# Kernel tuning notes

Hardware: AMD Instinct MI355X
Metric: run time of the kernel (lower is better)

## Reference

```python
import jax, jax.numpy as jnp
import numpy as np


def _shift_lr(t):
    # t: [B, L, H] -> (left, right) neighbor states with zero padding
    B, L, H = t.shape
    pad = jnp.zeros((B, 1, H), dtype=t.dtype)
    left = jnp.concatenate([pad, t[:, :-1, :]], axis=1)
    right = jnp.concatenate([t[:, 1:, :], pad], axis=1)
    return left, right


def setup_inputs() -> dict:
    key = jax.random.key(0)
    ks = jax.random.split(key, 7)
    B, L, H = 32, 2048, 256
    h_t = jax.random.normal(ks[0], (B, L, H), dtype=jnp.float32)
    x = jax.random.normal(ks[1], (B, L, H), dtype=jnp.float32)
    h_slot = jax.random.normal(ks[2], (B, L, H), dtype=jnp.float32)
    h_intent = jax.random.normal(ks[3], (B, L, H), dtype=jnp.float32)
    c_t = jax.random.normal(ks[4], (B, L, H), dtype=jnp.float32)
    # gate order: [i, o, f, l, r, u]; linear in = 6H, out = H
    Ws = jax.random.normal(ks[5], (6, 6 * H, H), dtype=jnp.float32) * 0.02
    bs = jnp.zeros((6, H), dtype=jnp.float32)
    return {"h_t": h_t, "x": x, "h_slot": h_slot, "h_intent": h_intent,
            "c_t": c_t, "Ws": Ws, "bs": bs}


def reference(h_t, x, h_slot, h_intent, c_t, Ws, bs):
    h_left, h_right = _shift_lr(h_t)
    # concat order: [h_mid, h_left, h_right, x, h_slot, h_intent] -> [B,L,6H]
    cat = jnp.concatenate([h_t, h_left, h_right, x, h_slot, h_intent], axis=-1)
    # one batched GEMM for all six gates: [6, B, L, H]
    gates = jnp.einsum('blc,gch->gblh', cat, Ws) + bs[:, None, None, :]
    i_t = jax.nn.sigmoid(gates[0])
    o_t = jax.nn.sigmoid(gates[1])
    f_t = jax.nn.sigmoid(gates[2])
    l_t = jax.nn.sigmoid(gates[3])
    r_t = jax.nn.sigmoid(gates[4])
    u_t = jnp.tanh(gates[5])
    # softmax across the 4 gates (axis 0 of the stack)
    soft = jax.nn.softmax(jnp.stack([i_t, f_t, l_t, r_t], axis=0), axis=0)
    i_t, f_t, l_t, r_t = soft[0], soft[1], soft[2], soft[3]
    c_left, c_right = _shift_lr(c_t)
    c_new = f_t * c_t + l_t * c_left + r_t * c_right + i_t * u_t
    h_new = o_t * jnp.tanh(c_new)
    return (h_new, c_new)
```

## Files before the change

kernel.cpp:

```cpp
#include <hip/hip_runtime.h>

typedef __attribute__((ext_vector_type(8))) short short8;
typedef __attribute__((ext_vector_type(4))) float f32x4;

#define BB 32
#define LL 2048
#define HH 256
#define MTOT (BB*LL)
#define KK 1536
#define HSIZE (MTOT*HH)

__device__ __forceinline__ unsigned short f2bf(float f){
    unsigned u = __builtin_bit_cast(unsigned, f);
    u += 0x7FFFu + ((u >> 16) & 1u);
    return (unsigned short)(u >> 16);
}
__device__ __forceinline__ unsigned pk2(float lo, float hi){
    return (unsigned)f2bf(lo) | ((unsigned)f2bf(hi) << 16);
}
__device__ __forceinline__ float sigm(float v){
    return 1.0f / (1.0f + __expf(-v));
}
__device__ __forceinline__ float ftanh(float v){
    v = fminf(fmaxf(v, -30.0f), 30.0f);
    float e = __expf(2.0f * v);
    return (e - 1.0f) / (e + 1.0f);
}

__global__ __launch_bounds__(256) void prep_bt(const float* __restrict__ Ws,
                                               unsigned short* __restrict__ Bt){
    __shared__ float tile[64][65];
    int bid = blockIdx.x;
    int kb = bid % 24; int tmp = bid / 24; int hb = tmp & 3; int g = tmp >> 2;
    int t = threadIdx.x;
    const float* src = Ws + (size_t)g * (KK * HH) + (size_t)(kb * 64) * HH + hb * 64;
    #pragma unroll
    for (int it = 0; it < 16; ++it){
        int e = it * 256 + t; int kk = e >> 6, hh = e & 63;
        tile[kk][hh] = src[(size_t)kk * HH + hh];
    }
    __syncthreads();
    unsigned short* dst = Bt + (size_t)(g * 256 + hb * 64) * KK + kb * 64;
    #pragma unroll
    for (int it = 0; it < 16; ++it){
        int e = it * 256 + t; int hh = e >> 6, kk = e & 63;
        dst[(size_t)hh * KK + kk] = f2bf(tile[kk][hh]);
    }
}

__global__ __launch_bounds__(512, 2) void slstm_fused(
    const float* __restrict__ h_t, const float* __restrict__ x,
    const float* __restrict__ h_slot, const float* __restrict__ h_intent,
    const float* __restrict__ c_t, const float* __restrict__ bs,
    const unsigned short* __restrict__ Bt, float* __restrict__ out)
{
    __shared__ unsigned short As[128 * 40];
    __shared__ unsigned short Bs[384 * 40];

    const int t    = threadIdx.x;
    const int wv   = t >> 6,  ln  = t & 63;
    const int rg   = wv >> 2, ht  = wv & 3;
    const int quad = ln >> 4, l16 = ln & 15;

    const int h_chunk = blockIdx.x & 3;
    const int m_block = blockIdx.x >> 2;
    const int h0      = h_chunk * 64;

    const int  arow = t >> 2;
    const int  akq  = (t & 3) << 3;
    const long mg   = (long)m_block * 128 + arow;
    const int  lseq = (int)(mg & (LL - 1));

    f32x4 acc[4][6] = {};

    for (int ks = 0; ks < 48; ++ks){
        {
            int c  = ks >> 3;
            int kk = ((ks & 7) << 5) + akq;
            const float* src; int sh;
            switch (c){
                case 0:  src = h_t;      sh =  0; break;
                case 1:  src = h_t;      sh = -1; break;
                case 2:  src = h_t;      sh =  1; break;
                case 3:  src = x;        sh =  0; break;
                case 4:  src = h_slot;   sh =  0; break;
                default: src = h_intent; sh =  0; break;
            }
            int sl = lseq + sh;
            float4 v0 = make_float4(0.f,0.f,0.f,0.f), v1 = v0;
            if ((unsigned)sl < (unsigned)LL){
                const float* p = src + ((mg + sh) * HH + kk);
                v0 = *(const float4*)p;
                v1 = *(const float4*)(p + 4);
            }
            uint4 w;
            w.x = pk2(v0.x, v0.y); w.y = pk2(v0.z, v0.w);
            w.z = pk2(v1.x, v1.y); w.w = pk2(v1.z, v1.w);
            *(uint4*)&As[arow * 40 + akq] = w;
        }
        #pragma unroll
        for (int i = 0; i < 3; ++i){
            int s   = i * 512 + t;
            int col = s >> 2;
            int kq  = (s & 3) << 3;
            int g   = col >> 6, hc = col & 63;
            const uint4 bv = *(const uint4*)(Bt + (size_t)(g * 256 + h0 + hc) * KK + ks * 32 + kq);
            *(uint4*)&Bs[col * 40 + kq] = bv;
        }
        __syncthreads();
        short8 a[4];
        #pragma unroll
        for (int mt = 0; mt < 4; ++mt)
            a[mt] = *(const short8*)&As[(rg * 64 + mt * 16 + l16) * 40 + quad * 8];
        #pragma unroll
        for (int g = 0; g < 6; ++g){
            short8 bfrag = *(const short8*)&Bs[(g * 64 + ht * 16 + l16) * 40 + quad * 8];
            #pragma unroll
            for (int mt = 0; mt < 4; ++mt)
                acc[mt][g] = __builtin_amdgcn_mfma_f32_16x16x32_bf16(a[mt], bfrag, acc[mt][g], 0, 0, 0);
        }
        __syncthreads();
    }

    const int h = h0 + ht * 16 + l16;
    float bias[6];
    #pragma unroll
    for (int g = 0; g < 6; ++g) bias[g] = bs[g * HH + h];

    #pragma unroll
    for (int mt = 0; mt < 4; ++mt){
        #pragma unroll
        for (int r = 0; r < 4; ++r){
            long row = (long)m_block * 128 + rg * 64 + mt * 16 + quad * 4 + r;
            int  ls  = (int)(row & (LL - 1));
            float gi = sigm(acc[mt][0][r] + bias[0]);
            float go = sigm(acc[mt][1][r] + bias[1]);
            float gf = sigm(acc[mt][2][r] + bias[2]);
            float gl = sigm(acc[mt][3][r] + bias[3]);
            float gr = sigm(acc[mt][4][r] + bias[4]);
            float gu = ftanh(acc[mt][5][r] + bias[5]);
            float ei = __expf(gi), ef = __expf(gf), el = __expf(gl), er = __expf(gr);
            float inv = 1.0f / (ei + ef + el + er);
            float cm  = c_t[row * HH + h];
            float clv = (ls > 0)      ? c_t[(row - 1) * HH + h] : 0.0f;
            float crv = (ls < LL - 1) ? c_t[(row + 1) * HH + h] : 0.0f;
            float cn  = (ef * cm + el * clv + er * crv + ei * gu) * inv;
            float hn  = go * ftanh(cn);
            out[row * HH + h]         = hn;
            out[HSIZE + row * HH + h] = cn;
        }
    }
}

extern "C" void kernel_launch(void* const* d_in, const int* in_sizes, int n_in,
                              void* d_out, int out_size, void* d_ws, size_t ws_size,
                              hipStream_t stream){
    const float* h_t      = (const float*)d_in[0];
    const float* x        = (const float*)d_in[1];
    const float* h_slot   = (const float*)d_in[2];
    const float* h_intent = (const float*)d_in[3];
    const float* c_t      = (const float*)d_in[4];
    const float* Ws       = (const float*)d_in[5];
    const float* bs       = (const float*)d_in[6];
    unsigned short* Bt    = (unsigned short*)d_ws;

    prep_bt<<<576, 256, 0, stream>>>(Ws, Bt);
    slstm_fused<<<2048, 512, 0, stream>>>(h_t, x, h_slot, h_intent, c_t, bs, Bt, (float*)d_out);
}
```

Measured before the change: 990.7 us.

## Double-buffer GEMM tiles with direct global-to-LDS B loads and XOR swizzle

Reworks the fused sLSTM GEMM main loop into a double-buffered pipeline. The next K-slice of activations is loaded into registers and the next weight slice is issued with global_load_lds before the current slice's MFMAs run, leaving one barrier per iteration. The weight prep kernel now writes B pre-tiled and XOR-swizzled so each K-slice is a contiguous chunk, and LDS rows drop the padding in favour of a matching swizzle. Block indices are also remapped to group blocks that share weight chunks. LDS use doubles, which may reduce occupancy, and correctness depends on the swizzled layouts staying consistent between the prep and fused kernels.

```diff
diff --git a/kernel.cpp b/kernel.cpp
--- a/kernel.cpp
+++ b/kernel.cpp
@@ -10,6 +10,8 @@
 #define KK 1536
 #define HSIZE (MTOT*HH)
 
+#define SWZ4(v) (((v) & 3) ^ (((v) >> 2) & 3))
+
 __device__ __forceinline__ unsigned short f2bf(float f){
     unsigned u = __builtin_bit_cast(unsigned, f);
     u += 0x7FFFu + ((u >> 16) & 1u);
@@ -25,6 +27,11 @@
     v = fminf(fmaxf(v, -30.0f), 30.0f);
     float e = __expf(2.0f * v);
     return (e - 1.0f) / (e + 1.0f);
+}
+__device__ __forceinline__ void gload_lds16(const void* g, void* l){
+    __builtin_amdgcn_global_load_lds(
+        (const __attribute__((address_space(1))) unsigned int*)g,
+        (__attribute__((address_space(3))) unsigned int*)l, 16, 0, 0);
 }
 
 __global__ __launch_bounds__(256) void prep_bt(const float* __restrict__ Ws,
@@ -40,11 +47,21 @@
         tile[kk][hh] = src[(size_t)kk * HH + hh];
     }
     __syncthreads();
-    unsigned short* dst = Bt + (size_t)(g * 256 + hb * 64) * KK + kb * 64;
-    #pragma unroll
-    for (int it = 0; it < 16; ++it){
-        int e = it * 256 + t; int hh = e >> 6, kk = e & 63;
-        dst[(size_t)hh * KK + kk] = f2bf(tile[kk][hh]);
+    #pragma unroll
+    for (int it = 0; it < 2; ++it){
+        int jj  = t;
+        int ksl = it;
+        int hc  = jj >> 2, qp = jj & 3;
+        int col = g * 64 + hc;
+        int q   = qp ^ SWZ4(col);
+        int kbase = ksl * 32 + q * 8;
+        unsigned wz[4];
+        #pragma unroll
+        for (int p = 0; p < 4; ++p)
+            wz[p] = pk2(tile[kbase + 2*p][hc], tile[kbase + 2*p + 1][hc]);
+        int ksg = kb * 2 + ksl;
+        size_t off = ((size_t)(hb * 48 + ksg) * 1536 + (size_t)g * 256 + jj) * 8;
+        *(uint4*)&Bt[off] = *(uint4*)wz;
     }
 }
 
@@ -54,71 +71,91 @@
     const float* __restrict__ c_t, const float* __restrict__ bs,
     const unsigned short* __restrict__ Bt, float* __restrict__ out)
 {
-    __shared__ unsigned short As[128 * 40];
-    __shared__ unsigned short Bs[384 * 40];
+    __shared__ __align__(16) unsigned short As[2][128 * 32];
+    __shared__ __align__(16) unsigned short Bs[2][384 * 32];
 
     const int t    = threadIdx.x;
     const int wv   = t >> 6,  ln  = t & 63;
     const int rg   = wv >> 2, ht  = wv & 3;
     const int quad = ln >> 4, l16 = ln & 15;
 
-    const int h_chunk = blockIdx.x & 3;
-    const int m_block = blockIdx.x >> 2;
+    const int rawb = blockIdx.x;
+    const int vb   = (rawb & 7) * 256 + (rawb >> 3);
+    const int h_chunk = vb & 3;
+    const int m_block = vb >> 2;
     const int h0      = h_chunk * 64;
 
     const int  arow = t >> 2;
-    const int  akq  = (t & 3) << 3;
+    const int  aq   = t & 3;
+    const int  akq  = aq << 3;
     const long mg   = (long)m_block * 128 + arow;
     const int  lseq = (int)(mg & (LL - 1));
+    const int  awq  = (aq ^ SWZ4(arow)) << 3;
+    const int  qa   = (quad ^ SWZ4(l16)) << 3;
+
+    const unsigned short* BtH = Bt + (size_t)h_chunk * 48 * 1536 * 8;
 
     f32x4 acc[4][6] = {};
 
+    float4 av0, av1;
+    auto stageA_issue = [&](int ks){
+        int c  = ks >> 3;
+        int kk = ((ks & 7) << 5) + akq;
+        const float* src; int sh;
+        switch (c){
+            case 0:  src = h_t;      sh =  0; break;
+            case 1:  src = h_t;      sh = -1; break;
+            case 2:  src = h_t;      sh =  1; break;
+            case 3:  src = x;        sh =  0; break;
+            case 4:  src = h_slot;   sh =  0; break;
+            default: src = h_intent; sh =  0; break;
+        }
+        int sl = lseq + sh;
+        av0 = make_float4(0.f,0.f,0.f,0.f); av1 = av0;
+        if ((unsigned)sl < (unsigned)LL){
+            const float* p = src + ((mg + sh) * HH + kk);
+            av0 = *(const float4*)p;
+            av1 = *(const float4*)(p + 4);
+        }
+    };
+    auto stageB = [&](int buf, int ks){
+        const unsigned short* gsrc = BtH + (size_t)ks * 1536 * 8;
+        #pragma unroll
+        for (int i = 0; i < 3; ++i){
+            gload_lds16(gsrc + (size_t)(i * 512 + t) * 8,
+                        &Bs[buf][(i * 512 + wv * 64) * 8]);
+        }
+    };
+    auto stageA_write = [&](int buf){
+        uint4 w;
+        w.x = pk2(av0.x, av0.y); w.y = pk2(av0.z, av0.w);
+        w.z = pk2(av1.x, av1.y); w.w = pk2(av1.z, av1.w);
+        *(uint4*)&As[buf][arow * 32 + awq] = w;
+    };
+
+    stageA_issue(0);
+    stageB(0, 0);
+    stageA_write(0);
+    __syncthreads();
+
     for (int ks = 0; ks < 48; ++ks){
-        {
-            int c  = ks >> 3;
-            int kk = ((ks & 7) << 5) + akq;
-            const float* src; int sh;
-            switch (c){
-                case 0:  src = h_t;      sh =  0; break;
-                case 1:  src = h_t;      sh = -1; break;
-                case 2:  src = h_t;      sh =  1; break;
-                case 3:  src = x;        sh =  0; break;
-                case 4:  src = h_slot;   sh =  0; break;
-                default: src = h_intent; sh =  0; break;
-            }
-            int sl = lseq + sh;
-            float4 v0 = make_float4(0.f,0.f,0.f,0.f), v1 = v0;
-            if ((unsigned)sl < (unsigned)LL){
-                const float* p = src + ((mg + sh) * HH + kk);
-                v0 = *(const float4*)p;
-                v1 = *(const float4*)(p + 4);
-            }
-            uint4 w;
-            w.x = pk2(v0.x, v0.y); w.y = pk2(v0.z, v0.w);
-            w.z = pk2(v1.x, v1.y); w.w = pk2(v1.z, v1.w);
-            *(uint4*)&As[arow * 40 + akq] = w;
-        }
-        #pragma unroll
-        for (int i = 0; i < 3; ++i){
-            int s   = i * 512 + t;
-            int col = s >> 2;
-            int kq  = (s & 3) << 3;
-            int g   = col >> 6, hc = col & 63;
-            const uint4 bv = *(const uint4*)(Bt + (size_t)(g * 256 + h0 + hc) * KK + ks * 32 + kq);
-            *(uint4*)&Bs[col * 40 + kq] = bv;
-        }
-        __syncthreads();
+        const int cur = ks & 1, nxt = cur ^ 1;
+        if (ks < 47){
+            stageA_issue(ks + 1);
+            stageB(nxt, ks + 1);
+        }
         short8 a[4];
         #pragma unroll
         for (int mt = 0; mt < 4; ++mt)
-            a[mt] = *(const short8*)&As[(rg * 64 + mt * 16 + l16) * 40 + quad * 8];
+            a[mt] = *(const short8*)&As[cur][(rg * 64 + mt * 16 + l16) * 32 + qa];
         #pragma unroll
         for (int g = 0; g < 6; ++g){
-            short8 bfrag = *(const short8*)&Bs[(g * 64 + ht * 16 + l16) * 40 + quad * 8];
+            short8 bfrag = *(const short8*)&Bs[cur][(g * 64 + ht * 16 + l16) * 32 + qa];
             #pragma unroll
             for (int mt = 0; mt < 4; ++mt)
                 acc[mt][g] = __builtin_amdgcn_mfma_f32_16x16x32_bf16(a[mt], bfrag, acc[mt][g], 0, 0, 0);
         }
+        if (ks < 47) stageA_write(nxt);
         __syncthreads();
     }
 
```

Measured after the change: 826.5 us. -16.6%, faster.
